# Kernel optimization log

Hardware: AMD Instinct MI355X
Metric: run time of the kernel (lower is better)

Reference implementation:

```python
import jax, jax.numpy as jnp
import numpy as np

N = 50000
E = 1600000
HID = 128
K = 2
EPS = 0.3


def setup_inputs() -> dict:
    key = jax.random.key(0)
    ks = jax.random.split(key, 8)
    x = jax.random.normal(ks[0], (N, 512), dtype=jnp.float32)
    edge_index = jax.random.randint(ks[1], (2, E), 0, N, dtype=jnp.int32)
    t1_w = jax.random.normal(ks[2], (HID, 512), dtype=jnp.float32) * (1.414 / np.sqrt(512))
    t1_b = jnp.zeros((HID,), dtype=jnp.float32)
    gate_w = jax.random.normal(ks[3], (K, 2 * HID), dtype=jnp.float32) * (1.414 / np.sqrt(2 * HID))
    gate_b = jnp.zeros((K,), dtype=jnp.float32)
    t2_w = jax.random.normal(ks[4], (40, HID), dtype=jnp.float32) * (1.414 / np.sqrt(HID))
    t2_b = jnp.zeros((40,), dtype=jnp.float32)
    return {"x": x, "edge_index": edge_index, "t1_w": t1_w, "t1_b": t1_b,
            "gate_w": gate_w, "gate_b": gate_b, "t2_w": t2_w, "t2_b": t2_b}


def reference(x, edge_index, t1_w, t1_b, gate_w, gate_b, t2_w, t2_b):
    row, col = edge_index[0], edge_index[1]
    # degree(row, num_nodes=N).clamp(min=1) ** -0.5
    deg = jax.ops.segment_sum(jnp.ones((E,), dtype=x.dtype), row, num_segments=N)
    norm_degree = jnp.clip(deg, 1.0) ** -0.5  # [N]

    h = jax.nn.relu(x @ t1_w.T + t1_b)  # [N, HID]
    raw = h
    for k in range(K):
        # gate(cat([h[row], h[col]], 1)) == h[row] @ W[:H] + h[col] @ W[H:]
        w_r, w_c = gate_w[k, :HID], gate_w[k, HID:]
        g = jnp.tanh(h[row] @ w_r + h[col] @ w_c + gate_b[k])  # [E]
        norm = g * norm_degree[row] * norm_degree[col]          # [E]
        # message: norm * x_j (x_j = h[row], source), scatter-add at col (target)
        agg = jax.ops.segment_sum(norm[:, None] * h[row], col, num_segments=N)
        h = EPS * raw + agg
    logits = h @ t2_w.T + t2_b  # [N, 40]
    return jax.nn.log_softmax(logits, axis=1)
```

## Files before the change

### kernel.cpp

```cpp
#include <hip/hip_runtime.h>
#include <hip/hip_bf16.h>
#include <hip/hip_fp16.h>

#define N_NODES 50000
#define N_EDGES 1600000
#define HIDDEN  128
#define EPS_C   0.3f
#define NWORDS  12500
#define CHUNK   12500
#define NCHUNK  128

typedef _Float16 f16x8 __attribute__((ext_vector_type(8)));
typedef _Float16 f16x4 __attribute__((ext_vector_type(4)));
typedef float    f32x16 __attribute__((ext_vector_type(16)));

__global__ __launch_bounds__(256) void k_hist(const int* __restrict__ ei, unsigned int* __restrict__ part) {
    __shared__ unsigned int hist[NWORDS];
    int b = blockIdx.x;
    int type  = b >> 7;
    int chunk = b & 127;
    const int* src = ei + (size_t)type * N_EDGES + (size_t)chunk * CHUNK;
    for (int i = threadIdx.x; i < NWORDS; i += 256) hist[i] = 0;
    __syncthreads();
    for (int i = threadIdx.x; i < CHUNK; i += 256) {
        int v = src[i];
        atomicAdd(&hist[v >> 2], 1u << ((v & 3) * 8));
    }
    __syncthreads();
    unsigned int* dst = part + ((size_t)type * NCHUNK + chunk) * NWORDS;
    for (int i = threadIdx.x; i < NWORDS; i += 256) dst[i] = hist[i];
}

__global__ __launch_bounds__(256) void k_reduce(const unsigned int* __restrict__ part,
                                                float* __restrict__ nd, int* __restrict__ cnt,
                                                unsigned short* __restrict__ cntpre) {
    int w = blockIdx.x * 256 + threadIdx.x;
    if (w >= NWORDS) return;
    unsigned int s0 = 0, s1 = 0, s2 = 0, s3 = 0;
    const unsigned int* dp = part + w;
    for (int b = 0; b < NCHUNK; ++b) {
        unsigned int v = dp[(size_t)b * NWORDS];
        s0 += v & 255u; s1 += (v >> 8) & 255u; s2 += (v >> 16) & 255u; s3 += v >> 24;
    }
    nd[4 * w + 0] = rsqrtf(fmaxf((float)s0, 1.f));
    nd[4 * w + 1] = rsqrtf(fmaxf((float)s1, 1.f));
    nd[4 * w + 2] = rsqrtf(fmaxf((float)s2, 1.f));
    nd[4 * w + 3] = rsqrtf(fmaxf((float)s3, 1.f));
    const unsigned int* cp = part + (size_t)NCHUNK * NWORDS + w;
    unsigned int r0 = 0, r1 = 0, r2 = 0, r3 = 0;
    for (int b = 0; b < NCHUNK; ++b) {
        size_t o = (size_t)b * N_NODES + 4 * w;
        *(ushort4*)&cntpre[o] = make_ushort4((unsigned short)r0, (unsigned short)r1,
                                             (unsigned short)r2, (unsigned short)r3);
        unsigned int v = cp[(size_t)b * NWORDS];
        r0 += v & 255u; r1 += (v >> 8) & 255u; r2 += (v >> 16) & 255u; r3 += v >> 24;
    }
    cnt[4 * w + 0] = (int)r0;
    cnt[4 * w + 1] = (int)r1;
    cnt[4 * w + 2] = (int)r2;
    cnt[4 * w + 3] = (int)r3;
}

__global__ __launch_bounds__(256) void k_scan_a(const int* __restrict__ cnt,
                                                int* __restrict__ out, int* __restrict__ partials) {
    __shared__ int sh[256];
    int t = threadIdx.x;
    int base = blockIdx.x * 1024 + t * 4;
    int v0 = (base + 0 < N_NODES) ? cnt[base + 0] : 0;
    int v1 = (base + 1 < N_NODES) ? cnt[base + 1] : 0;
    int v2 = (base + 2 < N_NODES) ? cnt[base + 2] : 0;
    int v3 = (base + 3 < N_NODES) ? cnt[base + 3] : 0;
    int s = v0 + v1 + v2 + v3;
    sh[t] = s;
    __syncthreads();
    for (int off = 1; off < 256; off <<= 1) {
        int add = (t >= off) ? sh[t - off] : 0;
        __syncthreads();
        sh[t] += add;
        __syncthreads();
    }
    int excl = sh[t] - s;
    if (t == 255) partials[blockIdx.x] = sh[255];
    if (base + 0 < N_NODES) out[base + 0] = excl;
    if (base + 1 < N_NODES) out[base + 1] = excl + v0;
    if (base + 2 < N_NODES) out[base + 2] = excl + v0 + v1;
    if (base + 3 < N_NODES) out[base + 3] = excl + v0 + v1 + v2;
}

__global__ void k_scan_b(int* partials, int* colptr, int nb) {
    if (threadIdx.x == 0 && blockIdx.x == 0) {
        int run = 0;
        for (int i = 0; i < nb; ++i) { int t = partials[i]; partials[i] = run; run += t; }
        colptr[N_NODES] = run;
    }
}

__global__ void k_scan_c(int* __restrict__ colptr, const int* __restrict__ partials) {
    int i = blockIdx.x * blockDim.x + threadIdx.x;
    if (i >= N_NODES) return;
    colptr[i] += partials[i >> 10];
}

__global__ __launch_bounds__(256) void k_scatter2(const int* __restrict__ ei, const int* __restrict__ colptr,
                                                  const unsigned short* __restrict__ cntpre,
                                                  int* __restrict__ csr) {
    __shared__ unsigned int rank[NWORDS];
    int b = blockIdx.x;
    for (int i = threadIdx.x; i < NWORDS; i += 256) rank[i] = 0;
    __syncthreads();
    const int* rs = ei + (size_t)b * CHUNK;
    const int* cs = ei + N_EDGES + (size_t)b * CHUNK;
    const unsigned short* pre = cntpre + (size_t)b * N_NODES;
    for (int i = threadIdx.x; i < CHUNK; i += 256) {
        int r = rs[i];
        int c = cs[i];
        unsigned int old = atomicAdd(&rank[c >> 2], 1u << ((c & 3) * 8));
        unsigned int lr = (old >> ((c & 3) * 8)) & 255u;
        int pos = colptr[c] + (int)pre[c] + (int)lr;
        csr[pos] = r;
    }
}

__global__ void k_cvt(const float4* __restrict__ src, __half2* __restrict__ dst, int n4) {
    int i = blockIdx.x * 256 + threadIdx.x;
    if (i >= n4) return;
    float4 v = src[i];
    dst[2 * i]     = __floats2half2_rn(v.x, v.y);
    dst[2 * i + 1] = __floats2half2_rn(v.z, v.w);
}

__global__ void k_cvtw(const float4* __restrict__ src, __half2* __restrict__ dst, int n4src, int n4tot) {
    int i = blockIdx.x * 256 + threadIdx.x;
    if (i >= n4tot) return;
    if (i < n4src) {
        float4 v = src[i];
        dst[2 * i]     = __floats2half2_rn(v.x, v.y);
        dst[2 * i + 1] = __floats2half2_rn(v.z, v.w);
    } else {
        __half2 z = __floats2half2_rn(0.f, 0.f);
        dst[2 * i]     = z;
        dst[2 * i + 1] = z;
    }
}

__global__ __launch_bounds__(256) void k_gemm1(const float* __restrict__ x, const _Float16* __restrict__ wh,
                                               const float* __restrict__ bias, float* __restrict__ h,
                                               _Float16* __restrict__ hb) {
    __shared__ _Float16 As[64 * 64];
    __shared__ _Float16 Bs[128 * 64];
    int t = threadIdx.x;
    int wave = t >> 6;
    int lane = t & 63;
    int lm   = lane & 31;
    int half = lane >> 5;
    int mstrip = wave & 1;
    int nstrip = wave >> 1;

    int m0  = blockIdx.x * 64;
    int wm0 = m0 + mstrip * 32;
    int n0  = nstrip * 64;

    int aidx[4], arow[4], ac4[4];
    int bidx, brow[4], bg[4];
#pragma unroll
    for (int i = 0; i < 4; ++i) {
        aidx[i] = i * 256 + t;
        arow[i] = aidx[i] >> 4;
        ac4[i]  = aidx[i] & 15;
        bidx    = i * 256 + t;
        brow[i] = bidx >> 3;
        bg[i]   = bidx & 7;
    }

    float4 pa[4];
    f16x8  pb[4];
#define LOAD_TILES(K0)                                                                    \
    {                                                                                     \
        _Pragma("unroll")                                                                 \
        for (int i = 0; i < 4; ++i) {                                                     \
            int gr = m0 + arow[i]; if (gr >= N_NODES) gr = N_NODES - 1;                   \
            pa[i] = *(const float4*)(x + (size_t)gr * 512 + (K0) + ac4[i] * 4);           \
            pb[i] = *(const f16x8*)(wh + (size_t)brow[i] * 512 + (K0) + bg[i] * 8);       \
        }                                                                                 \
    }

    f32x16 acc0, acc1;
#pragma unroll
    for (int i = 0; i < 16; ++i) { acc0[i] = 0.f; acc1[i] = 0.f; }

    int ar = mstrip * 32 + lm;
    int brA = n0 + lm;
    int brB = n0 + 32 + lm;

    LOAD_TILES(0);
    for (int k0 = 0; k0 < 512; k0 += 64) {
#pragma unroll
        for (int i = 0; i < 4; ++i) {
            f16x4 a;
            a[0] = (_Float16)pa[i].x; a[1] = (_Float16)pa[i].y;
            a[2] = (_Float16)pa[i].z; a[3] = (_Float16)pa[i].w;
            int g = ac4[i] >> 1;
            *(f16x4*)&As[arow[i] * 64 + (((g ^ (arow[i] & 7)) << 3)) + (ac4[i] & 1) * 4] = a;
            *(f16x8*)&Bs[brow[i] * 64 + ((bg[i] ^ (brow[i] & 7)) << 3)] = pb[i];
        }
        __syncthreads();
        if (k0 + 64 < 512) LOAD_TILES(k0 + 64);
#pragma unroll
        for (int kk = 0; kk < 4; ++kk) {
            int ag = kk * 2 + half;
            f16x8 av  = *(const f16x8*)&As[ar  * 64 + ((ag ^ (ar  & 7)) << 3)];
            f16x8 bv0 = *(const f16x8*)&Bs[brA * 64 + ((ag ^ (brA & 7)) << 3)];
            f16x8 bv1 = *(const f16x8*)&Bs[brB * 64 + ((ag ^ (brA & 7)) << 3)];
            acc0 = __builtin_amdgcn_mfma_f32_32x32x16_f16(av, bv0, acc0, 0, 0, 0);
            acc1 = __builtin_amdgcn_mfma_f32_32x32x16_f16(av, bv1, acc1, 0, 0, 0);
        }
        __syncthreads();
    }
#undef LOAD_TILES

    float bs0 = bias[n0 + lm];
    float bs1 = bias[n0 + 32 + lm];
#pragma unroll
    for (int reg = 0; reg < 16; ++reg) {
        int row = (reg & 3) + 8 * (reg >> 2) + 4 * half;
        int gm = wm0 + row;
        if (gm < N_NODES) {
            float v0 = fmaxf(acc0[reg] + bs0, 0.f);
            float v1 = fmaxf(acc1[reg] + bs1, 0.f);
            h[(size_t)gm * HIDDEN + n0 + lm]      = v0;
            h[(size_t)gm * HIDDEN + n0 + 32 + lm] = v1;
            hb[(size_t)gm * HIDDEN + n0 + lm]      = (_Float16)v0;
            hb[(size_t)gm * HIDDEN + n0 + 32 + lm] = (_Float16)v1;
        }
    }
}

__global__ __launch_bounds__(256) void k_dot(const float* __restrict__ h, const float* __restrict__ gw,
                                             const float* __restrict__ gb, const float* __restrict__ nd,
                                             int layer, float2* __restrict__ dn, float* __restrict__ dcb) {
    int node = blockIdx.x * 4 + (threadIdx.x >> 6);
    int lane = threadIdx.x & 63;
    if (node >= N_NODES) return;
    const float2* hv = (const float2*)h;
    float2 wr = ((const float2*)(gw + layer * 256))[lane];
    float2 wc = ((const float2*)(gw + layer * 256 + 128))[lane];
    float2 hc = hv[(size_t)node * 64 + lane];
    float a = hc.x * wr.x + hc.y * wr.y;
    float b = hc.x * wc.x + hc.y * wc.y;
#pragma unroll
    for (int off = 32; off >= 1; off >>= 1) {
        a += __shfl_xor(a, off, 64);
        b += __shfl_xor(b, off, 64);
    }
    if (lane == 0) {
        dn[node]  = make_float2(a, nd[node]);
        dcb[node] = b + gb[layer];
    }
}

__global__ __launch_bounds__(256) void k_edgew(const int* __restrict__ csr, const int* __restrict__ colptr,
                                               const float2* __restrict__ dn, const float* __restrict__ dcb,
                                               float* __restrict__ warr) {
    int node = blockIdx.x * 8 + (threadIdx.x >> 5);
    int sl   = threadIdx.x & 31;
    if (node >= N_NODES) return;
    float dc  = dcb[node];
    int beg = colptr[node], end = colptr[node + 1];
    for (int p = beg + sl; p < end; p += 32) {
        int r = csr[p];
        float2 v = dn[r];
        float xx = v.x + dc;
        float t = __expf(2.0f * xx);
        float g = 1.0f - 2.0f / (t + 1.0f);
        warr[p] = g * v.y;
    }
}

__global__ __launch_bounds__(256) void k_prop(const __half2* __restrict__ hb, const float* __restrict__ raw,
                                              const int* __restrict__ colptr, const int* __restrict__ csr,
                                              const float* __restrict__ warr, const float* __restrict__ nd,
                                              float* __restrict__ hn, __half2* __restrict__ hbn) {
    int lane = threadIdx.x & 63;
    int node = __builtin_amdgcn_readfirstlane(blockIdx.x * 4 + (threadIdx.x >> 6));
    int beg = __builtin_amdgcn_readfirstlane(colptr[node]);
    int end = __builtin_amdgcn_readfirstlane(colptr[node + 1]);
    float acc0 = 0.f, acc1 = 0.f;
    int p = beg;
    for (; p + 8 <= end; p += 8) {
        int r0 = csr[p + 0], r1 = csr[p + 1], r2 = csr[p + 2], r3 = csr[p + 3];
        int r4 = csr[p + 4], r5 = csr[p + 5], r6 = csr[p + 6], r7 = csr[p + 7];
        float w0 = warr[p + 0], w1 = warr[p + 1], w2 = warr[p + 2], w3 = warr[p + 3];
        float w4 = warr[p + 4], w5 = warr[p + 5], w6 = warr[p + 6], w7 = warr[p + 7];
        __half2 v0 = hb[(size_t)r0 * 64 + lane];
        __half2 v1 = hb[(size_t)r1 * 64 + lane];
        __half2 v2 = hb[(size_t)r2 * 64 + lane];
        __half2 v3 = hb[(size_t)r3 * 64 + lane];
        __half2 v4 = hb[(size_t)r4 * 64 + lane];
        __half2 v5 = hb[(size_t)r5 * 64 + lane];
        __half2 v6 = hb[(size_t)r6 * 64 + lane];
        __half2 v7 = hb[(size_t)r7 * 64 + lane];
        acc0 = fmaf(w0, __low2float(v0), acc0);  acc1 = fmaf(w0, __high2float(v0), acc1);
        acc0 = fmaf(w1, __low2float(v1), acc0);  acc1 = fmaf(w1, __high2float(v1), acc1);
        acc0 = fmaf(w2, __low2float(v2), acc0);  acc1 = fmaf(w2, __high2float(v2), acc1);
        acc0 = fmaf(w3, __low2float(v3), acc0);  acc1 = fmaf(w3, __high2float(v3), acc1);
        acc0 = fmaf(w4, __low2float(v4), acc0);  acc1 = fmaf(w4, __high2float(v4), acc1);
        acc0 = fmaf(w5, __low2float(v5), acc0);  acc1 = fmaf(w5, __high2float(v5), acc1);
        acc0 = fmaf(w6, __low2float(v6), acc0);  acc1 = fmaf(w6, __high2float(v6), acc1);
        acc0 = fmaf(w7, __low2float(v7), acc0);  acc1 = fmaf(w7, __high2float(v7), acc1);
    }
    for (; p < end; ++p) {
        int r = csr[p];
        float w = warr[p];
        __half2 v = hb[(size_t)r * 64 + lane];
        acc0 = fmaf(w, __low2float(v), acc0);
        acc1 = fmaf(w, __high2float(v), acc1);
    }
    float ndc = nd[node];
    float2 rw = ((const float2*)raw)[(size_t)node * 64 + lane];
    float2 o;
    o.x = fmaf(EPS_C, rw.x, ndc * acc0);
    o.y = fmaf(EPS_C, rw.y, ndc * acc1);
    if (hn)  ((float2*)hn)[(size_t)node * 64 + lane] = o;
    if (hbn) hbn[(size_t)node * 64 + lane] = __floats2half2_rn(o.x, o.y);
}

__global__ __launch_bounds__(256) void k_out(const _Float16* __restrict__ h16, const _Float16* __restrict__ w2h,
                                             const float* __restrict__ b2, float* __restrict__ out) {
    int wave = threadIdx.x >> 6;
    int lane = threadIdx.x & 63;
    int lm   = lane & 31;
    int half = lane >> 5;

    int wm0 = blockIdx.x * 128 + wave * 32;
    int m   = wm0 + lm;
    int mc  = (m < N_NODES) ? m : (N_NODES - 1);

    const _Float16* arow  = h16 + (size_t)mc * HIDDEN + half * 8;
    const _Float16* brow0 = w2h + (size_t)lm * HIDDEN + half * 8;
    const _Float16* brow1 = w2h + (size_t)(32 + lm) * HIDDEN + half * 8;

    f32x16 acc0, acc1;
#pragma unroll
    for (int i = 0; i < 16; ++i) { acc0[i] = 0.f; acc1[i] = 0.f; }

#pragma unroll
    for (int k0 = 0; k0 < 128; k0 += 16) {
        f16x8 av = *(const f16x8*)(arow  + k0);
        f16x8 b0 = *(const f16x8*)(brow0 + k0);
        f16x8 b1 = *(const f16x8*)(brow1 + k0);
        acc0 = __builtin_amdgcn_mfma_f32_32x32x16_f16(av, b0, acc0, 0, 0, 0);
        acc1 = __builtin_amdgcn_mfma_f32_32x32x16_f16(av, b1, acc1, 0, 0, 0);
    }

    float bj0 = b2[lm];
    float bj1 = (lm < 8) ? b2[32 + lm] : 0.f;

#pragma unroll
    for (int reg = 0; reg < 16; ++reg) {
        int row = (reg & 3) + 8 * (reg >> 2) + 4 * half;
        float v0 = acc0[reg] + bj0;
        float v1 = (lm < 8) ? (acc1[reg] + bj1) : -INFINITY;
        float mx = fmaxf(v0, v1);
#pragma unroll
        for (int off = 16; off >= 1; off >>= 1) mx = fmaxf(mx, __shfl_xor(mx, off, 64));
        float s = __expf(v0 - mx) + ((lm < 8) ? __expf(v1 - mx) : 0.f);
#pragma unroll
        for (int off = 16; off >= 1; off >>= 1) s += __shfl_xor(s, off, 64);
        float ls = __logf(s) + mx;
        int gm = wm0 + row;
        if (gm < N_NODES) {
            out[(size_t)gm * 40 + lm] = v0 - ls;
            if (lm < 8) out[(size_t)gm * 40 + 32 + lm] = v1 - ls;
        }
    }
}

extern "C" void kernel_launch(void* const* d_in, const int* in_sizes, int n_in,
                              void* d_out, int out_size, void* d_ws, size_t ws_size,
                              hipStream_t stream) {
    const float* x   = (const float*)d_in[0];
    const int*   ei  = (const int*)  d_in[1];
    const float* t1w = (const float*)d_in[2];
    const float* t1b = (const float*)d_in[3];
    const float* gw  = (const float*)d_in[4];
    const float* gb  = (const float*)d_in[5];
    const float* w2  = (const float*)d_in[6];
    const float* b2  = (const float*)d_in[7];
    float* out = (float*)d_out;

    char* p = (char*)d_ws;
    int*    colptr   = (int*)p;    p += (size_t)(N_NODES + 64) * 4;
    int*    partials = (int*)p;    p += 256 * 4;
    float*  nd       = (float*)p;  p += (size_t)N_NODES * 4;
    int*    cnt      = (int*)p;    p += (size_t)N_NODES * 4;
    float*  dcb      = (float*)p;  p += (size_t)N_NODES * 4;
    float2* dn       = (float2*)p; p += (size_t)N_NODES * 8;
    int*    csr      = (int*)p;    p += (size_t)N_EDGES * 4;
    float*  warr     = (float*)p;  p += (size_t)N_EDGES * 4;
    _Float16* wh     = (_Float16*)p; p += (size_t)HIDDEN * 512 * 2;
    _Float16* w2h    = (_Float16*)p; p += (size_t)64 * HIDDEN * 2;
    char* q = p;
    unsigned int*   part   = (unsigned int*)q;
    unsigned short* cntpre = (unsigned short*)(q + (size_t)2 * NCHUNK * NWORDS * 4);
    __half2* hb0 = (__half2*)p; p += (size_t)N_NODES * 64 * 4;
    __half2* hb1 = (__half2*)p; p += (size_t)N_NODES * 64 * 4;
    __half2* hb2 = (__half2*)p; p += (size_t)N_NODES * 64 * 4;
    float*  h0   = (float*)p;   p += (size_t)N_NODES * HIDDEN * 4;
    float*  h1   = (float*)p;   p += (size_t)N_NODES * HIDDEN * 4;

    k_hist<<<2 * NCHUNK, 256, 0, stream>>>(ei, part);
    k_reduce<<<(NWORDS + 255) / 256, 256, 0, stream>>>(part, nd, cnt, cntpre);
    int nb = (N_NODES + 1023) / 1024;
    k_scan_a<<<nb, 256, 0, stream>>>(cnt, colptr, partials);
    k_scan_b<<<1, 64, 0, stream>>>(partials, colptr, nb);
    k_scan_c<<<(N_NODES + 255) / 256, 256, 0, stream>>>(colptr, partials);
    k_scatter2<<<NCHUNK, 256, 0, stream>>>(ei, colptr, cntpre, csr);

    k_cvt<<<(16384 + 255) / 256, 256, 0, stream>>>((const float4*)t1w, (__half2*)wh, 16384);
    k_cvtw<<<8, 256, 0, stream>>>((const float4*)w2, (__half2*)w2h, 40 * HIDDEN / 4, 64 * HIDDEN / 4);
    k_gemm1<<<(N_NODES + 63) / 64, 256, 0, stream>>>(x, wh, t1b, h0, (_Float16*)hb0);

    k_dot  <<<(N_NODES + 3) / 4, 256, 0, stream>>>(h0, gw, gb, nd, 0, dn, dcb);
    k_edgew<<<(N_NODES + 7) / 8, 256, 0, stream>>>(csr, colptr, dn, dcb, warr);
    k_prop <<<(N_NODES + 3) / 4, 256, 0, stream>>>(hb0, h0, colptr, csr, warr, nd, h1, hb1);

    k_dot  <<<(N_NODES + 3) / 4, 256, 0, stream>>>(h1, gw, gb, nd, 1, dn, dcb);
    k_edgew<<<(N_NODES + 7) / 8, 256, 0, stream>>>(csr, colptr, dn, dcb, warr);
    k_prop <<<(N_NODES + 3) / 4, 256, 0, stream>>>(hb1, h0, colptr, csr, warr, nd, (float*)nullptr, hb2);

    k_out<<<(N_NODES + 127) / 128, 256, 0, stream>>>((const _Float16*)hb2, w2h, b2, out);
}
```

Before: 470.2 us.

## Drop fp32 hidden buffers and fuse next-layer gate dot into propagation

The fp32 copies of the hidden state are no longer written. The gate dot products and the residual term now read the fp16 buffers instead. The second layer's gate dot product is computed inside the first propagation kernel from the freshly computed output, which removes one kernel launch and one full pass over the hidden state. This cuts memory traffic by about 25 MB per fp32 buffer, at the cost of feeding fp16-rounded values into the gate and the residual term.

```diff
diff --git a/kernel.cpp b/kernel.cpp
--- a/kernel.cpp
+++ b/kernel.cpp
@@ -144,8 +144,7 @@
 }
 
 __global__ __launch_bounds__(256) void k_gemm1(const float* __restrict__ x, const _Float16* __restrict__ wh,
-                                               const float* __restrict__ bias, float* __restrict__ h,
-                                               _Float16* __restrict__ hb) {
+                                               const float* __restrict__ bias, _Float16* __restrict__ hb) {
     __shared__ _Float16 As[64 * 64];
     __shared__ _Float16 Bs[128 * 64];
     int t = threadIdx.x;
@@ -227,24 +226,21 @@
         if (gm < N_NODES) {
             float v0 = fmaxf(acc0[reg] + bs0, 0.f);
             float v1 = fmaxf(acc1[reg] + bs1, 0.f);
-            h[(size_t)gm * HIDDEN + n0 + lm]      = v0;
-            h[(size_t)gm * HIDDEN + n0 + 32 + lm] = v1;
             hb[(size_t)gm * HIDDEN + n0 + lm]      = (_Float16)v0;
             hb[(size_t)gm * HIDDEN + n0 + 32 + lm] = (_Float16)v1;
         }
     }
 }
 
-__global__ __launch_bounds__(256) void k_dot(const float* __restrict__ h, const float* __restrict__ gw,
+__global__ __launch_bounds__(256) void k_dot(const __half2* __restrict__ hb, const float* __restrict__ gw,
                                              const float* __restrict__ gb, const float* __restrict__ nd,
                                              int layer, float2* __restrict__ dn, float* __restrict__ dcb) {
     int node = blockIdx.x * 4 + (threadIdx.x >> 6);
     int lane = threadIdx.x & 63;
     if (node >= N_NODES) return;
-    const float2* hv = (const float2*)h;
     float2 wr = ((const float2*)(gw + layer * 256))[lane];
     float2 wc = ((const float2*)(gw + layer * 256 + 128))[lane];
-    float2 hc = hv[(size_t)node * 64 + lane];
+    float2 hc = __half22float2(hb[(size_t)node * 64 + lane]);
     float a = hc.x * wr.x + hc.y * wr.y;
     float b = hc.x * wc.x + hc.y * wc.y;
 #pragma unroll
@@ -276,10 +272,12 @@
     }
 }
 
-__global__ __launch_bounds__(256) void k_prop(const __half2* __restrict__ hb, const float* __restrict__ raw,
+__global__ __launch_bounds__(256) void k_prop(const __half2* __restrict__ hb, const __half2* __restrict__ rawh,
                                               const int* __restrict__ colptr, const int* __restrict__ csr,
                                               const float* __restrict__ warr, const float* __restrict__ nd,
-                                              float* __restrict__ hn, __half2* __restrict__ hbn) {
+                                              const float* __restrict__ gw_next, const float* __restrict__ gb_next,
+                                              float2* __restrict__ dn, float* __restrict__ dcb,
+                                              __half2* __restrict__ hbn) {
     int lane = threadIdx.x & 63;
     int node = __builtin_amdgcn_readfirstlane(blockIdx.x * 4 + (threadIdx.x >> 6));
     int beg = __builtin_amdgcn_readfirstlane(colptr[node]);
@@ -316,12 +314,26 @@
         acc1 = fmaf(w, __high2float(v), acc1);
     }
     float ndc = nd[node];
-    float2 rw = ((const float2*)raw)[(size_t)node * 64 + lane];
+    float2 rw = __half22float2(rawh[(size_t)node * 64 + lane]);
     float2 o;
     o.x = fmaf(EPS_C, rw.x, ndc * acc0);
     o.y = fmaf(EPS_C, rw.y, ndc * acc1);
-    if (hn)  ((float2*)hn)[(size_t)node * 64 + lane] = o;
-    if (hbn) hbn[(size_t)node * 64 + lane] = __floats2half2_rn(o.x, o.y);
+    hbn[(size_t)node * 64 + lane] = __floats2half2_rn(o.x, o.y);
+    if (gw_next) {
+        float2 wr = ((const float2*)gw_next)[lane];
+        float2 wc = ((const float2*)(gw_next + 128))[lane];
+        float a = o.x * wr.x + o.y * wr.y;
+        float b = o.x * wc.x + o.y * wc.y;
+#pragma unroll
+        for (int off = 32; off >= 1; off >>= 1) {
+            a += __shfl_xor(a, off, 64);
+            b += __shfl_xor(b, off, 64);
+        }
+        if (lane == 0) {
+            dn[node]  = make_float2(a, ndc);
+            dcb[node] = b + gb_next[0];
+        }
+    }
 }
 
 __global__ __launch_bounds__(256) void k_out(const _Float16* __restrict__ h16, const _Float16* __restrict__ w2h,
@@ -405,8 +417,6 @@
     __half2* hb0 = (__half2*)p; p += (size_t)N_NODES * 64 * 4;
     __half2* hb1 = (__half2*)p; p += (size_t)N_NODES * 64 * 4;
     __half2* hb2 = (__half2*)p; p += (size_t)N_NODES * 64 * 4;
-    float*  h0   = (float*)p;   p += (size_t)N_NODES * HIDDEN * 4;
-    float*  h1   = (float*)p;   p += (size_t)N_NODES * HIDDEN * 4;
 
     k_hist<<<2 * NCHUNK, 256, 0, stream>>>(ei, part);
     k_reduce<<<(NWORDS + 255) / 256, 256, 0, stream>>>(part, nd, cnt, cntpre);
@@ -418,15 +428,17 @@
 
     k_cvt<<<(16384 + 255) / 256, 256, 0, stream>>>((const float4*)t1w, (__half2*)wh, 16384);
     k_cvtw<<<8, 256, 0, stream>>>((const float4*)w2, (__half2*)w2h, 40 * HIDDEN / 4, 64 * HIDDEN / 4);
-    k_gemm1<<<(N_NODES + 63) / 64, 256, 0, stream>>>(x, wh, t1b, h0, (_Float16*)hb0);
-
-    k_dot  <<<(N_NODES + 3) / 4, 256, 0, stream>>>(h0, gw, gb, nd, 0, dn, dcb);
+    k_gemm1<<<(N_NODES + 63) / 64, 256, 0, stream>>>(x, wh, t1b, (_Float16*)hb0);
+
+    k_dot  <<<(N_NODES + 3) / 4, 256, 0, stream>>>(hb0, gw, gb, nd, 0, dn, dcb);
     k_edgew<<<(N_NODES + 7) / 8, 256, 0, stream>>>(csr, colptr, dn, dcb, warr);
-    k_prop <<<(N_NODES + 3) / 4, 256, 0, stream>>>(hb0, h0, colptr, csr, warr, nd, h1, hb1);
-
-    k_dot  <<<(N_NODES + 3) / 4, 256, 0, stream>>>(h1, gw, gb, nd, 1, dn, dcb);
+    k_prop <<<(N_NODES + 3) / 4, 256, 0, stream>>>(hb0, hb0, colptr, csr, warr, nd,
+                                                   gw + 256, gb + 1, dn, dcb, hb1);
+
     k_edgew<<<(N_NODES + 7) / 8, 256, 0, stream>>>(csr, colptr, dn, dcb, warr);
-    k_prop <<<(N_NODES + 3) / 4, 256, 0, stream>>>(hb1, h0, colptr, csr, warr, nd, (float*)nullptr, hb2);
+    k_prop <<<(N_NODES + 3) / 4, 256, 0, stream>>>(hb1, hb0, colptr, csr, warr, nd,
+                                                   (const float*)nullptr, (const float*)nullptr,
+                                                   (float2*)nullptr, (float*)nullptr, hb2);
 
     k_out<<<(N_NODES + 127) / 128, 256, 0, stream>>>((const _Float16*)hb2, w2h, b2, out);
 }
```

Result: faster. 450.9 us (-4.1%).
